# Kernel optimization log

Measured on AMD Instinct MI355X. Metric: run time of the kernel, lower is better.

## Reference

```python
import jax, jax.numpy as jnp
import numpy as np

def setup_inputs() -> dict:
    key = jax.random.key(0)
    k1, k2, k3, k4 = jax.random.split(key, 4)
    B, T, C, D = 4, 4096, 1024, 128
    x = jax.random.normal(k1, (B, T, C), dtype=jnp.float32)
    Wq = jax.random.normal(k2, (C, D), dtype=jnp.float32) * (C ** -0.5)
    Wk = jax.random.normal(k3, (C, D), dtype=jnp.float32) * (C ** -0.5)
    Wv = jax.random.normal(k4, (C, D), dtype=jnp.float32) * (C ** -0.5)
    return {"x": x, "Wq": Wq, "Wk": Wk, "Wv": Wv}

def reference(x, Wq, Wk, Wv):
    # x: [B,T,C]; Wq/Wk/Wv: [C,D] (nn.Linear bias=False => x @ W)
    B, T, C = x.shape
    q = jnp.einsum('btc,cd->btd', x, Wq)  # [B,T,D]
    k = jnp.einsum('btc,cd->btd', x, Wk)
    v = jnp.einsum('btc,cd->btd', x, Wv)
    dk = q.shape[-1]
    scale = dk ** -0.5
    w = jnp.einsum('btd,bsd->bts', q, k) * scale  # [B,T,T]
    causal = jnp.tril(jnp.ones((T, T), dtype=bool))
    w = jnp.where(causal, w, -jnp.inf)
    w = jax.nn.softmax(w, axis=-1)
    # dropout p=0.0 => identity
    attention = jnp.einsum('bts,bsd->btd', w, v)  # [B,T,D]
    return attention
```

## Files before the change

### kernel.cpp

```cpp
#include <hip/hip_runtime.h>
#include <stdint.h>

typedef __bf16 bf16_t;
typedef bf16_t bf16x8 __attribute__((ext_vector_type(8)));
typedef float f32x4 __attribute__((ext_vector_type(4)));
typedef float f32x16 __attribute__((ext_vector_type(16)));
typedef unsigned short us8 __attribute__((ext_vector_type(8)));
typedef unsigned short us4 __attribute__((ext_vector_type(4)));
typedef unsigned int u32x4 __attribute__((ext_vector_type(4)));

#define B_ 4
#define T_ 4096
#define C_ 1024
#define D_ 128

#define NCHUNK_PB 144
#define QSCALE 0.12751744f
#define M0 14.0f

__device__ __forceinline__ uint16_t f2bf(float f) {
    union { float f; uint32_t u; } v; v.f = f;
    uint32_t u = v.u;
    uint32_t r = (u + 0x7fffu + ((u >> 16) & 1u)) >> 16;
    return (uint16_t)r;
}

__device__ __forceinline__ uint16_t bfru(float f) {
    return (uint16_t)((__float_as_uint(f) + 0x8000u) >> 16);
}

__device__ __forceinline__ float bf2f(uint16_t u) {
    return __uint_as_float((uint32_t)u << 16);
}

__device__ __forceinline__ uint32_t cvtpk(float a, float b) {
    uint32_t r;
    asm("v_cvt_pk_bf16_f32 %0, %1, %2" : "=v"(r) : "v"(a), "v"(b));
    return r;
}

__device__ __forceinline__ void pl32swap(uint32_t& a, uint32_t& b) {
    asm("v_permlane32_swap_b32 %0, %1" : "+v"(a), "+v"(b));
}

__device__ __forceinline__ void gload_lds16(const void* g, void* l) {
    __builtin_amdgcn_global_load_lds(
        (const __attribute__((address_space(1))) void*)g,
        (__attribute__((address_space(3))) void*)l, 16, 0, 0);
}

__global__ __launch_bounds__(256) void prep_w(const float* __restrict__ Wq,
                                              const float* __restrict__ Wk,
                                              const float* __restrict__ Wv,
                                              uint16_t* __restrict__ WT) {
    int idx = blockIdx.x * 256 + threadIdx.x;
    if (idx >= 3 * D_ * C_) return;
    int w   = idx / (D_ * C_);
    int rem = idx - w * (D_ * C_);
    int n   = rem / C_;
    int k   = rem - n * C_;
    const float* W = (w == 0) ? Wq : (w == 1) ? Wk : Wv;
    WT[idx] = f2bf(W[(size_t)k * D_ + n]);
}

#define GST 72

__global__ __launch_bounds__(256) void qkv_gemm(const float* __restrict__ x,
                                                const uint16_t* __restrict__ WT,
                                                uint16_t* __restrict__ qb,
                                                uint16_t* __restrict__ kb,
                                                uint16_t* __restrict__ vT) {
    __shared__ __align__(16) uint16_t A_lds[64 * GST];
    __shared__ __align__(16) uint16_t W_lds[128 * GST];

    int tid  = threadIdx.x;
    int lane = tid & 63;
    int wave = tid >> 6;
    int quad = lane >> 4;
    int lx   = lane & 15;
    int wm   = wave >> 1, wn = wave & 1;

    int bx   = blockIdx.x;
    int wsel = bx % 3;
    int m0   = (bx / 3) * 64;
    const uint16_t* Wp = WT + (size_t)wsel * (D_ * C_);

    f32x4 acc[2][4];
    for (int mf = 0; mf < 2; mf++)
        for (int nf = 0; nf < 4; nf++)
            acc[mf][nf] = (f32x4){0.f, 0.f, 0.f, 0.f};

    int arow = tid >> 2, acb = (tid & 3) * 16;
    int wrow = tid >> 1, wcb = (tid & 1) * 32;

    for (int k0 = 0; k0 < C_; k0 += 64) {
        {
            const float* xp = x + (size_t)(m0 + arow) * C_ + k0 + acb;
            uint32_t d[8];
#pragma unroll
            for (int j = 0; j < 4; j++) {
                float4 f = *(const float4*)(xp + j * 4);
                uint32_t u0 = __float_as_uint(f.x) + 0x8000u;
                uint32_t u1 = __float_as_uint(f.y) + 0x8000u;
                uint32_t u2 = __float_as_uint(f.z) + 0x8000u;
                uint32_t u3 = __float_as_uint(f.w) + 0x8000u;
                d[2 * j]     = __builtin_amdgcn_perm(u1, u0, 0x07060302);
                d[2 * j + 1] = __builtin_amdgcn_perm(u3, u2, 0x07060302);
            }
            *(u32x4*)&A_lds[arow * GST + acb]     = (u32x4){d[0], d[1], d[2], d[3]};
            *(u32x4*)&A_lds[arow * GST + acb + 8] = (u32x4){d[4], d[5], d[6], d[7]};
        }
        {
            const uint16_t* wp = Wp + (size_t)wrow * C_ + k0 + wcb;
#pragma unroll
            for (int i = 0; i < 4; i++)
                *(us8*)&W_lds[wrow * GST + wcb + i * 8] = *(const us8*)(wp + i * 8);
        }
        __syncthreads();

#pragma unroll
        for (int kc = 0; kc < 2; kc++) {
            bf16x8 af[2];
#pragma unroll
            for (int mf = 0; mf < 2; mf++)
                af[mf] = *(const bf16x8*)&A_lds[(wm * 32 + mf * 16 + lx) * GST + kc * 32 + quad * 8];
#pragma unroll
            for (int nf = 0; nf < 4; nf++) {
                bf16x8 bf = *(const bf16x8*)&W_lds[(wn * 64 + nf * 16 + lx) * GST + kc * 32 + quad * 8];
                acc[0][nf] = __builtin_amdgcn_mfma_f32_16x16x32_bf16(af[0], bf, acc[0][nf], 0, 0, 0);
                acc[1][nf] = __builtin_amdgcn_mfma_f32_16x16x32_bf16(af[1], bf, acc[1][nf], 0, 0, 0);
            }
        }
        __syncthreads();
    }

    int mrow0 = m0 + wm * 32 + quad * 4;
    if (wsel == 2) {
#pragma unroll
        for (int mf = 0; mf < 2; mf++) {
            int mbase = mrow0 + mf * 16;
            int batch = mbase >> 12;
            int t     = mbase & 4095;
#pragma unroll
            for (int nf = 0; nf < 4; nf++) {
                int n = wn * 64 + nf * 16 + lx;
                us4 pv;
#pragma unroll
                for (int r = 0; r < 4; r++) pv[r] = bfru(acc[mf][nf][r]);
                *(us4*)&vT[(size_t)batch * D_ * T_ + (size_t)n * T_ + t] = pv;
            }
        }
    } else {
        uint16_t* dst = (wsel == 0) ? qb : kb;
        float sc = (wsel == 0) ? QSCALE : 1.0f;
#pragma unroll
        for (int mf = 0; mf < 2; mf++)
#pragma unroll
            for (int nf = 0; nf < 4; nf++) {
                int n = wn * 64 + nf * 16 + lx;
#pragma unroll
                for (int r = 0; r < 4; r++)
                    dst[(size_t)(mrow0 + mf * 16 + r) * D_ + n] = bfru(acc[mf][nf][r] * sc);
            }
    }
}

__global__ __launch_bounds__(256, 2) void attn(const uint16_t* __restrict__ qb,
                                               const uint16_t* __restrict__ kb,
                                               const uint16_t* __restrict__ vT,
                                               uint16_t* __restrict__ part,
                                               float* __restrict__ ml) {
    __shared__ __align__(16) uint16_t K_lds[2][64 * 128];
    __shared__ __align__(16) uint16_t V_lds[2][128 * 64];

    int tid  = threadIdx.x;
    int lane = tid & 63;
    int wave = tid >> 6;
    int q31  = lane & 31;
    int hi   = lane >> 5;

    int batch = blockIdx.x & 3;
    int L     = NCHUNK_PB - 1 - (blockIdx.x >> 2);
    int a = 0;
    while (a < 7 && 2 * (a + 1) * (a + 2) <= L) a++;
    int rem   = L - 2 * a * (a + 1);
    int jt    = 4 * a + rem / (a + 1);
    int chunk = rem - (rem / (a + 1)) * (a + 1);
    int lidx  = batch * NCHUNK_PB + L;

    int q0     = jt * 128;
    int st0    = chunk * 8;
    int ntiles = min(8, 2 * jt + 2 - st0);

    auto issue_kv = [&](int bi, int tile) {
        int s0i = tile * 64;
        const uint16_t* kB = kb + (size_t)(batch * T_ + s0i) * D_;
#pragma unroll
        for (int j = 0; j < 4; j++) {
            int row = wave * 16 + j * 4 + (lane >> 4);
            int gch = (lane & 15) ^ (row & 7);
            gload_lds16(kB + (size_t)row * D_ + gch * 8,
                        &K_lds[bi][(wave * 16 + j * 4) * 128]);
        }
        const uint16_t* vB = vT + (size_t)batch * D_ * T_ + s0i;
#pragma unroll
        for (int j = 0; j < 4; j++) {
            int row = wave * 32 + j * 8 + (lane >> 3);
            int gch = (lane & 7) ^ (row & 7);
            gload_lds16(vB + (size_t)row * T_ + gch * 8,
                        &V_lds[bi][(wave * 32 + j * 8) * 64]);
        }
    };

    bf16x8 qf[8];
    {
        const uint16_t* qp = qb + (size_t)(batch * T_ + q0 + wave * 32 + q31) * D_ + hi * 8;
#pragma unroll
        for (int kc = 0; kc < 8; kc++) qf[kc] = *(const bf16x8*)(qp + kc * 16);
    }

    f32x16 o[4];
#pragma unroll
    for (int i = 0; i < 4; i++)
#pragma unroll
        for (int r = 0; r < 16; r++) o[i][r] = 0.f;
    float lsum = 0.f;

    issue_kv(0, st0);
    int cur = 0;

    for (int it = 0; it < ntiles; it++) {
        int s0 = (st0 + it) * 64;
        __syncthreads();
        if (it + 1 < ntiles) issue_kv(cur ^ 1, st0 + it + 1);

        f32x16 st[2];
#pragma unroll
        for (int nt = 0; nt < 2; nt++)
#pragma unroll
            for (int r = 0; r < 16; r++) st[nt][r] = 0.f;
        __builtin_amdgcn_s_setprio(1);
#pragma unroll
        for (int kc = 0; kc < 8; kc++)
#pragma unroll
            for (int nt = 0; nt < 2; nt++) {
                int row = nt * 32 + q31;
                bf16x8 kf = *(const bf16x8*)&K_lds[cur][row * 128 + (((kc * 2 + hi) ^ (row & 7)) * 8)];
                st[nt] = __builtin_amdgcn_mfma_f32_32x32x16_bf16(kf, qf[kc], st[nt], 0, 0, 0);
            }
        __builtin_amdgcn_s_setprio(0);

        if (st0 + it >= 2 * jt) {
            int qg = q0 + wave * 32 + q31;
#pragma unroll
            for (int nt = 0; nt < 2; nt++)
#pragma unroll
                for (int r = 0; r < 16; r++) {
                    int sg = s0 + nt * 32 + (r & 3) + 8 * (r >> 2) + 4 * hi;
                    if (sg > qg) st[nt][r] = -INFINITY;
                }
        }

#pragma unroll
        for (int nt = 0; nt < 2; nt++)
#pragma unroll
            for (int r = 0; r < 16; r++) {
                st[nt][r] = exp2f(st[nt][r] - M0);
                lsum += st[nt][r];
            }

        bf16x8 pa[4];
#pragma unroll
        for (int nt = 0; nt < 2; nt++) {
            uint32_t x0 = cvtpk(st[nt][0],  st[nt][1]);
            uint32_t x1 = cvtpk(st[nt][2],  st[nt][3]);
            uint32_t y0 = cvtpk(st[nt][4],  st[nt][5]);
            uint32_t y1 = cvtpk(st[nt][6],  st[nt][7]);
            pl32swap(x0, y0);
            pl32swap(x1, y1);
            u32x4 w0 = (u32x4){x0, x1, y0, y1};
            pa[2 * nt] = *(bf16x8*)&w0;
            uint32_t z0 = cvtpk(st[nt][8],  st[nt][9]);
            uint32_t z1 = cvtpk(st[nt][10], st[nt][11]);
            uint32_t t0 = cvtpk(st[nt][12], st[nt][13]);
            uint32_t t1 = cvtpk(st[nt][14], st[nt][15]);
            pl32swap(z0, t0);
            pl32swap(z1, t1);
            u32x4 w1 = (u32x4){z0, z1, t0, t1};
            pa[2 * nt + 1] = *(bf16x8*)&w1;
        }

        __builtin_amdgcn_s_setprio(1);
#pragma unroll
        for (int sb = 0; sb < 4; sb++)
#pragma unroll
            for (int ntd = 0; ntd < 4; ntd++) {
                int row = ntd * 32 + q31;
                bf16x8 vf = *(const bf16x8*)&V_lds[cur][row * 64 + (((sb * 2 + hi) ^ (row & 7)) * 8)];
                o[ntd] = __builtin_amdgcn_mfma_f32_32x32x16_bf16(pa[sb], vf, o[ntd], 0, 0, 0);
            }
        __builtin_amdgcn_s_setprio(0);
        cur ^= 1;
    }

    lsum += __shfl_xor(lsum, 32, 64);

    uint16_t* pp = part + (size_t)lidx * (128 * 128);
#pragma unroll
    for (int ntd = 0; ntd < 4; ntd++)
#pragma unroll
        for (int r = 0; r < 16; r++) {
            int lrow = wave * 32 + (r & 3) + 8 * (r >> 2) + 4 * hi;
            pp[lrow * 128 + ntd * 32 + q31] = bfru(o[ntd][r]);
        }
    if (lane < 32)
        ml[(size_t)lidx * 128 + wave * 32 + q31] = lsum;
}

__global__ __launch_bounds__(256) void combine(const uint16_t* __restrict__ part,
                                               const float* __restrict__ ml,
                                               float* __restrict__ out) {
    int bidx  = blockIdx.x;
    int half  = bidx & 1;
    int jt    = (bidx >> 1) & 31;
    int batch = bidx >> 6;
    int a     = jt >> 2;
    int base  = batch * NCHUNK_PB + 2 * a * (a + 1) + (jt - 4 * a) * (a + 1);
    int nch   = a + 1;

    int tid  = threadIdx.x;
    int lrow = tid >> 1;
    int c0   = half * 64 + (tid & 1) * 32;

    float Lsum = 0.f;
    f32x4 acc[8];
#pragma unroll
    for (int i = 0; i < 8; i++) acc[i] = (f32x4){0.f, 0.f, 0.f, 0.f};

    for (int c = 0; c < nch; c++) {
        Lsum += ml[(size_t)(base + c) * 128 + lrow];
        const uint16_t* p = part + (size_t)(base + c) * (128 * 128) + lrow * 128 + c0;
#pragma unroll
        for (int i = 0; i < 4; i++) {
            us8 v = *(const us8*)(p + i * 8);
#pragma unroll
            for (int j = 0; j < 8; j++)
                acc[i * 2 + (j >> 2)][j & 3] += bf2f(v[j]);
        }
    }
    float inv = 1.f / Lsum;
    size_t row = (size_t)(batch * T_ + jt * 128 + lrow);
#pragma unroll
    for (int i = 0; i < 8; i++)
        *(f32x4*)(out + row * 128 + c0 + i * 4) = acc[i] * inv;
}

extern "C" void kernel_launch(void* const* d_in, const int* in_sizes, int n_in,
                              void* d_out, int out_size, void* d_ws, size_t ws_size,
                              hipStream_t stream) {
    const float* x  = (const float*)d_in[0];
    const float* Wq = (const float*)d_in[1];
    const float* Wk = (const float*)d_in[2];
    const float* Wv = (const float*)d_in[3];
    float* out = (float*)d_out;

    uint16_t* ws = (uint16_t*)d_ws;
    uint16_t* qb = ws;
    uint16_t* kb = qb + (size_t)16384 * 128;
    uint16_t* vT = kb + (size_t)16384 * 128;
    uint16_t* WT = vT + (size_t)16384 * 128;
    uint16_t* part = WT + (size_t)3 * D_ * C_;
    float* ml = (float*)(part + (size_t)4 * NCHUNK_PB * 128 * 128);

    prep_w<<<dim3((3 * D_ * C_ + 255) / 256), dim3(256), 0, stream>>>(Wq, Wk, Wv, WT);
    qkv_gemm<<<dim3(3 * (16384 / 64)), dim3(256), 0, stream>>>(x, WT, qb, kb, vT);
    attn<<<dim3(B_ * NCHUNK_PB), dim3(256), 0, stream>>>(qb, kb, vT, part, ml);
    combine<<<dim3(B_ * 32 * 2), dim3(256), 0, stream>>>(part, ml, out);
}
```

Measured before the change: 185.6 us.

## Fuse Q/K/V projections into one GEMM block with async double-buffered loads

Each block now computes all three Q, K and V projections for its 64-row tile, so x is read from global memory once instead of three times. Tiles are loaded straight into LDS with asynchronous global-to-LDS copies using an XOR swizzle and double buffering, and x stays fp32 in LDS until it is converted to bf16 at fragment load. The cost is fewer blocks (256 blocks of 512 threads) and more accumulator registers per thread, which may lower occupancy and parallelism.

```diff
diff --git a/kernel.cpp b/kernel.cpp
--- a/kernel.cpp
+++ b/kernel.cpp
@@ -63,105 +63,102 @@
     WT[idx] = f2bf(W[(size_t)k * D_ + n]);
 }
 
-#define GST 72
-
-__global__ __launch_bounds__(256) void qkv_gemm(const float* __restrict__ x,
-                                                const uint16_t* __restrict__ WT,
-                                                uint16_t* __restrict__ qb,
-                                                uint16_t* __restrict__ kb,
-                                                uint16_t* __restrict__ vT) {
-    __shared__ __align__(16) uint16_t A_lds[64 * GST];
-    __shared__ __align__(16) uint16_t W_lds[128 * GST];
+__global__ __launch_bounds__(512, 2) void qkv_fused(const float* __restrict__ x,
+                                                    const uint16_t* __restrict__ WT,
+                                                    uint16_t* __restrict__ qb,
+                                                    uint16_t* __restrict__ kb,
+                                                    uint16_t* __restrict__ vT) {
+    __shared__ __align__(16) float    A_lds[2][64 * 32];
+    __shared__ __align__(16) uint16_t W_lds[2][192 * 64];
 
     int tid  = threadIdx.x;
     int lane = tid & 63;
     int wave = tid >> 6;
     int quad = lane >> 4;
     int lx   = lane & 15;
-    int wm   = wave >> 1, wn = wave & 1;
-
-    int bx   = blockIdx.x;
-    int wsel = bx % 3;
-    int m0   = (bx / 3) * 64;
-    const uint16_t* Wp = WT + (size_t)wsel * (D_ * C_);
-
-    f32x4 acc[2][4];
-    for (int mf = 0; mf < 2; mf++)
-        for (int nf = 0; nf < 4; nf++)
-            acc[mf][nf] = (f32x4){0.f, 0.f, 0.f, 0.f};
-
-    int arow = tid >> 2, acb = (tid & 3) * 16;
-    int wrow = tid >> 1, wcb = (tid & 1) * 32;
-
-    for (int k0 = 0; k0 < C_; k0 += 64) {
+    int wm   = wave >> 2;
+    int wn   = wave & 3;
+
+    int m0 = blockIdx.x * 64;
+
+    auto issue_ab = [&](int bi, int k0) {
         {
-            const float* xp = x + (size_t)(m0 + arow) * C_ + k0 + acb;
-            uint32_t d[8];
-#pragma unroll
-            for (int j = 0; j < 4; j++) {
-                float4 f = *(const float4*)(xp + j * 4);
-                uint32_t u0 = __float_as_uint(f.x) + 0x8000u;
-                uint32_t u1 = __float_as_uint(f.y) + 0x8000u;
-                uint32_t u2 = __float_as_uint(f.z) + 0x8000u;
-                uint32_t u3 = __float_as_uint(f.w) + 0x8000u;
-                d[2 * j]     = __builtin_amdgcn_perm(u1, u0, 0x07060302);
-                d[2 * j + 1] = __builtin_amdgcn_perm(u3, u2, 0x07060302);
-            }
-            *(u32x4*)&A_lds[arow * GST + acb]     = (u32x4){d[0], d[1], d[2], d[3]};
-            *(u32x4*)&A_lds[arow * GST + acb + 8] = (u32x4){d[4], d[5], d[6], d[7]};
-        }
-        {
-            const uint16_t* wp = Wp + (size_t)wrow * C_ + k0 + wcb;
-#pragma unroll
-            for (int i = 0; i < 4; i++)
-                *(us8*)&W_lds[wrow * GST + wcb + i * 8] = *(const us8*)(wp + i * 8);
-        }
+            int row = wave * 8 + (lane >> 3);
+            int gch = (lane & 7) ^ (row & 7);
+            gload_lds16(x + (size_t)(m0 + row) * C_ + k0 + gch * 4,
+                        &A_lds[bi][(wave * 8) * 32]);
+        }
+#pragma unroll
+        for (int c = 0; c < 3; c++) {
+            int fl  = wave * 24 + c * 8 + (lane >> 3);
+            int gch = (lane & 7) ^ (fl & 7);
+            int wsel = fl >> 6;
+            int n    = 2 * (fl & 63) + (gch >> 2);
+            gload_lds16(WT + (size_t)wsel * (D_ * C_) + (size_t)n * C_ + k0 + (gch & 3) * 8,
+                        &W_lds[bi][(wave * 24 + c * 8) * 64]);
+        }
+    };
+
+    f32x4 acc[3][2][2];
+#pragma unroll
+    for (int w = 0; w < 3; w++)
+#pragma unroll
+        for (int mf = 0; mf < 2; mf++)
+#pragma unroll
+            for (int nf = 0; nf < 2; nf++)
+                acc[w][mf][nf] = (f32x4){0.f, 0.f, 0.f, 0.f};
+
+    issue_ab(0, 0);
+    int cur = 0;
+
+    for (int k0 = 0; k0 < C_; k0 += 32) {
         __syncthreads();
-
-#pragma unroll
-        for (int kc = 0; kc < 2; kc++) {
-            bf16x8 af[2];
-#pragma unroll
-            for (int mf = 0; mf < 2; mf++)
-                af[mf] = *(const bf16x8*)&A_lds[(wm * 32 + mf * 16 + lx) * GST + kc * 32 + quad * 8];
-#pragma unroll
-            for (int nf = 0; nf < 4; nf++) {
-                bf16x8 bf = *(const bf16x8*)&W_lds[(wn * 64 + nf * 16 + lx) * GST + kc * 32 + quad * 8];
-                acc[0][nf] = __builtin_amdgcn_mfma_f32_16x16x32_bf16(af[0], bf, acc[0][nf], 0, 0, 0);
-                acc[1][nf] = __builtin_amdgcn_mfma_f32_16x16x32_bf16(af[1], bf, acc[1][nf], 0, 0, 0);
-            }
-        }
-        __syncthreads();
-    }
-
-    int mrow0 = m0 + wm * 32 + quad * 4;
-    if (wsel == 2) {
+        if (k0 + 32 < C_) issue_ab(cur ^ 1, k0 + 32);
+
+        bf16x8 af[2];
 #pragma unroll
         for (int mf = 0; mf < 2; mf++) {
-            int mbase = mrow0 + mf * 16;
-            int batch = mbase >> 12;
-            int t     = mbase & 4095;
-#pragma unroll
-            for (int nf = 0; nf < 4; nf++) {
-                int n = wn * 64 + nf * 16 + lx;
-                us4 pv;
-#pragma unroll
-                for (int r = 0; r < 4; r++) pv[r] = bfru(acc[mf][nf][r]);
-                *(us4*)&vT[(size_t)batch * D_ * T_ + (size_t)n * T_ + t] = pv;
-            }
-        }
-    } else {
-        uint16_t* dst = (wsel == 0) ? qb : kb;
-        float sc = (wsel == 0) ? QSCALE : 1.0f;
-#pragma unroll
-        for (int mf = 0; mf < 2; mf++)
-#pragma unroll
-            for (int nf = 0; nf < 4; nf++) {
-                int n = wn * 64 + nf * 16 + lx;
-#pragma unroll
-                for (int r = 0; r < 4; r++)
-                    dst[(size_t)(mrow0 + mf * 16 + r) * D_ + n] = bfru(acc[mf][nf][r] * sc);
-            }
+            int arow = wm * 32 + mf * 16 + lx;
+            const float* ar = &A_lds[cur][arow * 32];
+            f32x4 a0 = *(const f32x4*)&ar[((2 * quad) ^ (arow & 7)) * 4];
+            f32x4 a1 = *(const f32x4*)&ar[((2 * quad + 1) ^ (arow & 7)) * 4];
+            u32x4 w = (u32x4){cvtpk(a0[0], a0[1]), cvtpk(a0[2], a0[3]),
+                              cvtpk(a1[0], a1[1]), cvtpk(a1[2], a1[3])};
+            af[mf] = *(bf16x8*)&w;
+        }
+
+#pragma unroll
+        for (int wsel = 0; wsel < 3; wsel++)
+#pragma unroll
+            for (int nf = 0; nf < 2; nf++) {
+                int n  = wn * 32 + nf * 16 + lx;
+                int rp = n >> 1;
+                int ch = ((n & 1) * 4 + quad) ^ (rp & 7);
+                bf16x8 wf = *(const bf16x8*)&W_lds[cur][(wsel * 64 + rp) * 64 + ch * 8];
+                acc[wsel][0][nf] = __builtin_amdgcn_mfma_f32_16x16x32_bf16(af[0], wf, acc[wsel][0][nf], 0, 0, 0);
+                acc[wsel][1][nf] = __builtin_amdgcn_mfma_f32_16x16x32_bf16(af[1], wf, acc[wsel][1][nf], 0, 0, 0);
+            }
+        cur ^= 1;
+    }
+
+#pragma unroll
+    for (int mf = 0; mf < 2; mf++) {
+        int mrow0 = m0 + wm * 32 + mf * 16 + quad * 4;
+        int batch = mrow0 >> 12;
+        int t     = mrow0 & 4095;
+#pragma unroll
+        for (int nf = 0; nf < 2; nf++) {
+            int n = wn * 32 + nf * 16 + lx;
+#pragma unroll
+            for (int r = 0; r < 4; r++) {
+                qb[(size_t)(mrow0 + r) * D_ + n] = bfru(acc[0][mf][nf][r] * QSCALE);
+                kb[(size_t)(mrow0 + r) * D_ + n] = bfru(acc[1][mf][nf][r]);
+            }
+            us4 pv;
+#pragma unroll
+            for (int r = 0; r < 4; r++) pv[r] = bfru(acc[2][mf][nf][r]);
+            *(us4*)&vT[(size_t)batch * D_ * T_ + (size_t)n * T_ + t] = pv;
+        }
     }
 }
 
@@ -373,7 +370,7 @@
     float* ml = (float*)(part + (size_t)4 * NCHUNK_PB * 128 * 128);
 
     prep_w<<<dim3((3 * D_ * C_ + 255) / 256), dim3(256), 0, stream>>>(Wq, Wk, Wv, WT);
-    qkv_gemm<<<dim3(3 * (16384 / 64)), dim3(256), 0, stream>>>(x, WT, qb, kb, vT);
+    qkv_fused<<<dim3(16384 / 64), dim3(512), 0, stream>>>(x, WT, qb, kb, vT);
     attn<<<dim3(B_ * NCHUNK_PB), dim3(256), 0, stream>>>(qb, kb, vT, part, ml);
     combine<<<dim3(B_ * 32 * 2), dim3(256), 0, stream>>>(part, ml, out);
 }
```

Result: no change. 186.3 us (+0.4%).
